# Kernel tuning notes

Measured on AMD Instinct MI355X. Metric: run time of the kernel, lower is better.

## Reference

```python
import jax, jax.numpy as jnp
import numpy as np

EPS = 1e-6

def _ln(x):
    mu = jnp.mean(x, -1, keepdims=True)
    var = jnp.mean((x - mu) ** 2, -1, keepdims=True)
    return (x - mu) / jnp.sqrt(var + EPS)

def _mha(q_in, k_in, v_in, w, mask, h):
    # w: [4, d, d] = (Wq, Wk, Wv, Wo), stored as [in, out]
    b, sq, d = q_in.shape
    dk = d // h
    q = (q_in @ w[0]).reshape(b, sq, h, dk)
    k = (k_in @ w[1]).reshape(b, k_in.shape[1], h, dk)
    v = (v_in @ w[2]).reshape(b, v_in.shape[1], h, dk)
    scores = jnp.einsum('bqhd,bkhd->bhqk', q, k) / np.sqrt(dk).astype(q.dtype)
    if mask is not None:
        scores = jnp.where(mask, scores, jnp.asarray(-jnp.inf, scores.dtype))
    attn = jax.nn.softmax(scores, -1)
    out = jnp.einsum('bhqk,bkhd->bqhd', attn, v).reshape(b, sq, d)
    return out @ w[3]

def setup_inputs() -> dict:
    B, S, D, V, NL, ML = 8, 256, 1024, 32000, 6, 256
    ks = jax.random.split(jax.random.key(0), 8)
    sc = 0.02
    return {
        'memory': jax.random.normal(ks[0], (B, S, D), jnp.float32),
        'gold_tokens': jax.random.randint(ks[1], (B, ML), 0, V),
        'attn_w': jax.random.normal(ks[2], (NL, 2, 4, D, D), jnp.float32) * sc,
        'ffn_w1': jax.random.normal(ks[3], (NL, D, 4 * D), jnp.float32) * sc,
        'ffn_w2': jax.random.normal(ks[4], (NL, 4 * D, D), jnp.float32) * sc,
        'tok_emb': jax.random.normal(ks[5], (V, D - ML), jnp.float32) * sc,
        'sos': jax.random.normal(ks[6], (D,), jnp.float32),
        'gen_w': jax.random.normal(ks[7], (D, V), jnp.float32) * sc,
    }

def reference(memory, gold_tokens, attn_w, ffn_w1, ffn_w2, tok_emb, sos, gen_w):
    B = memory.shape[0]
    ML = gold_tokens.shape[1]          # max_length == decoder len
    NL = attn_w.shape[0]
    H = 8
    temperature = 1.0
    # embedding: token embed (dim d-ML) concat one-hot position (dim ML)
    dec_input = gold_tokens[:, :-1]                      # [B, ML-1]
    tok = tok_emb[dec_input]                             # [B, ML-1, D-ML]
    pos = jax.nn.one_hot(jnp.arange(ML - 1), ML, dtype=tok.dtype)  # [ML-1, ML]
    pos = jnp.broadcast_to(pos[None], (B, ML - 1, ML))
    emb = jnp.concatenate([tok, pos], -1)                # [B, ML-1, D]
    sos_tok = jnp.broadcast_to(sos[None, None, :], (B, 1, sos.shape[0]))
    x = jnp.concatenate([sos_tok, emb], 1)               # [B, ML, D]
    causal = jnp.tril(jnp.ones((ML, ML), bool))[None, None]  # True = keep
    for l in range(NL):
        h1 = _ln(x)
        x = x + _mha(h1, h1, h1, attn_w[l, 0], causal, H)       # self-attn
        x = x + _mha(_ln(x), memory, memory, attn_w[l, 1], None, H)  # cross-attn (raw memory keys/values)
        h2 = _ln(x)
        x = x + jax.nn.relu(h2 @ ffn_w1[l]) @ ffn_w2[l]
    logits = _ln(x) @ gen_w
    return jax.nn.log_softmax(logits / temperature, -1)
```

## Files before the change

kernel.cpp:

```cpp
#include <hip/hip_runtime.h>
#include <hip/hip_bf16.h>
#include <cstdint>
#include <cstddef>

using bf16 = __hip_bfloat16;
typedef __attribute__((ext_vector_type(8))) short bf16x8;
typedef __attribute__((ext_vector_type(4))) float f32x4;

#define DEV static __device__ __forceinline__

DEV unsigned short f2bf(float f) {
    bf16 h = __float2bfloat16(f);
    return __builtin_bit_cast(unsigned short, h);
}

typedef const __attribute__((address_space(1))) void* as1cv;
typedef __attribute__((address_space(3))) void* as3v;

DEV void load_lds16(const void* g, void* l) {
    __builtin_amdgcn_global_load_lds((as1cv)g, (as3v)l, 16, 0, 0);
}

template<int EPI>
__global__ __launch_bounds__(256)
void gemm_k(const bf16* __restrict__ Ag, const bf16* __restrict__ Bg,
            void* __restrict__ Cg,
            int Mdim, int Ndim, int Kdim,
            int lda, int ldb, int ldc,
            int Hdim, long aZ1, long aZ2, long bZ1, long bZ2,
            long cZ1, long cZ2, float scale,
            float* __restrict__ pp, const bf16* __restrict__ Ag2, int ySplitA)
{
    __shared__ __align__(16) char lds[32768];
    char* ldsA = lds;
    char* ldsB = lds + 16384;

    const int t = threadIdx.x;
    const int wave = t >> 6, lane = t & 63;
    const int wr = wave >> 1, wc = wave & 1;
    const int lo = lane & 15, hi = lane >> 4;

    const int bx2 = blockIdx.x, by2 = blockIdx.y;
    const int m0 = bx2 * 128, n0 = by2 * 128;
    const int z = blockIdx.z;
    const int z1 = z / Hdim, z2 = z - z1 * Hdim;

    const bf16* Abase = (by2 >= ySplitA) ? Ag2 : Ag;
    const bf16* A = Abase + (size_t)z1 * aZ1 + (size_t)z2 * aZ2;
    const bf16* B = Bg + (size_t)z1 * bZ1 + (size_t)z2 * bZ2;

    f32x4 acc[4][4];
#pragma unroll
    for (int m = 0; m < 4; ++m)
#pragma unroll
        for (int n = 0; n < 4; ++n)
            acc[m][n] = f32x4{0.f, 0.f, 0.f, 0.f};

    const int nk = Kdim >> 6;
    for (int kt = 0; kt < nk; ++kt) {
        const int k0 = kt << 6;
#pragma unroll
        for (int i = 0; i < 4; ++i) {
            int u = i * 256 + t;
            int row = u >> 3;
            int cb = (u & 7) ^ (row & 7);
            load_lds16(A + (size_t)(m0 + row) * lda + (k0 + cb * 8),
                       ldsA + i * 4096 + wave * 1024);
        }
#pragma unroll
        for (int i = 0; i < 4; ++i) {
            int u = i * 256 + t;
            int row = u >> 3;
            int cb = (u & 7) ^ (row & 7);
            load_lds16(B + (size_t)(n0 + row) * ldb + (k0 + cb * 8),
                       ldsB + i * 4096 + wave * 1024);
        }
        __syncthreads();
#pragma unroll
        for (int kk = 0; kk < 2; ++kk) {
            bf16x8 af[4], bfr[4];
#pragma unroll
            for (int m = 0; m < 4; ++m) {
                int row = wr * 64 + m * 16 + lo;
                int cbyte = ((kk << 6) + (hi << 4)) ^ ((row & 7) << 4);
                af[m] = *(const bf16x8*)(ldsA + row * 128 + cbyte);
            }
#pragma unroll
            for (int n = 0; n < 4; ++n) {
                int row = wc * 64 + n * 16 + lo;
                int cbyte = ((kk << 6) + (hi << 4)) ^ ((row & 7) << 4);
                bfr[n] = *(const bf16x8*)(ldsB + row * 128 + cbyte);
            }
#pragma unroll
            for (int m = 0; m < 4; ++m)
#pragma unroll
                for (int n = 0; n < 4; ++n)
                    acc[m][n] = __builtin_amdgcn_mfma_f32_16x16x32_bf16(
                        af[m], bfr[n], acc[m][n], 0, 0, 0);
        }
        __syncthreads();
    }

    const int rb = hi << 2;
    if (EPI == 0 || EPI == 1) {
        unsigned short* C = (unsigned short*)Cg + (size_t)z1 * cZ1 + (size_t)z2 * cZ2;
#pragma unroll
        for (int m = 0; m < 4; ++m)
#pragma unroll
            for (int n = 0; n < 4; ++n)
#pragma unroll
                for (int r = 0; r < 4; ++r) {
                    int row = m0 + wr * 64 + m * 16 + rb + r;
                    int col = n0 + wc * 64 + n * 16 + lo;
                    float v = acc[m][n][r];
                    if (EPI == 1) v = fmaxf(v, 0.f);
                    C[(size_t)row * ldc + col] = f2bf(v);
                }
    } else if (EPI == 5) {
        float* C = (float*)Cg + (size_t)z1 * cZ1 + (size_t)z2 * cZ2;
#pragma unroll
        for (int m = 0; m < 4; ++m)
#pragma unroll
            for (int n = 0; n < 4; ++n)
#pragma unroll
                for (int r = 0; r < 4; ++r) {
                    int row = m0 + wr * 64 + m * 16 + rb + r;
                    int col = n0 + wc * 64 + n * 16 + lo;
                    atomicAdd(&C[(size_t)row * ldc + col], acc[m][n][r]);
                }
    } else {
        float* C = (float*)Cg + (size_t)z1 * cZ1 + (size_t)z2 * cZ2;
#pragma unroll
        for (int m = 0; m < 4; ++m)
#pragma unroll
            for (int n = 0; n < 4; ++n)
#pragma unroll
                for (int r = 0; r < 4; ++r) {
                    int row = m0 + wr * 64 + m * 16 + rb + r;
                    int col = n0 + wc * 64 + n * 16 + lo;
                    C[(size_t)row * ldc + col] = acc[m][n][r] * scale;
                }
        float* lp = (float*)lds;
#pragma unroll
        for (int m = 0; m < 4; ++m)
#pragma unroll
            for (int r = 0; r < 4; ++r) {
                float vm = -3.4e38f;
#pragma unroll
                for (int n = 0; n < 4; ++n) vm = fmaxf(vm, acc[m][n][r] * scale);
#pragma unroll
                for (int o = 1; o < 16; o <<= 1) vm = fmaxf(vm, __shfl_xor(vm, o));
                float vs = 0.f;
#pragma unroll
                for (int n = 0; n < 4; ++n) vs += __expf(acc[m][n][r] * scale - vm);
#pragma unroll
                for (int o = 1; o < 16; o <<= 1) vs += __shfl_xor(vs, o);
                if (lo == 0) {
                    int rl = wr * 64 + m * 16 + rb + r;
                    lp[(rl * 2 + wc) * 2 + 0] = vm;
                    lp[(rl * 2 + wc) * 2 + 1] = vs;
                }
            }
        __syncthreads();
        if (t < 128) {
            float ma = lp[(t * 2 + 0) * 2], sa = lp[(t * 2 + 0) * 2 + 1];
            float mb = lp[(t * 2 + 1) * 2], sb = lp[(t * 2 + 1) * 2 + 1];
            float mm = fmaxf(ma, mb);
            float ss = sa * __expf(ma - mm) + sb * __expf(mb - mm);
            size_t idx2 = ((size_t)(m0 + t) * gridDim.y + by2) * 2;
            pp[idx2] = mm; pp[idx2 + 1] = ss;
        }
    }
}

template<int CAUSAL>
__global__ __launch_bounds__(256)
void attn_k(const bf16* __restrict__ qkv, const bf16* __restrict__ VT,
            bf16* __restrict__ attno)
{
    __shared__ __align__(16) char ldsK[16384];
    __shared__ __align__(16) char ldsP[8192];
    const float SC = 0.088388347648318447f;

    const int t = threadIdx.x, w = t >> 6, lane = t & 63;
    const int lo = lane & 15, hi = lane >> 4;
    const int qb = blockIdx.x, z = blockIdx.y;
    const int b = z >> 3, h = z & 7;
    const int qr0 = qb * 64 + w * 16;

    const unsigned short* Qg = (const unsigned short*)qkv + (size_t)(b * 256) * 3072 + h * 128;
    const unsigned short* Kg = Qg + 1024;
    const unsigned short* VTz = (const unsigned short*)VT + (size_t)z * 32768;

    bf16x8 qf[4];
#pragma unroll
    for (int ks = 0; ks < 4; ++ks)
        qf[ks] = *(const bf16x8*)(Qg + (size_t)(qr0 + lo) * 3072 + ks * 32 + hi * 8);

    f32x4 accO[8];
#pragma unroll
    for (int n2 = 0; n2 < 8; ++n2) accO[n2] = f32x4{0.f, 0.f, 0.f, 0.f};
    float mrun[4], lrun[4];
#pragma unroll
    for (int r = 0; r < 4; ++r) { mrun[r] = -3.0e38f; lrun[r] = 0.f; }

    const int nkt = CAUSAL ? (qb + 1) : 4;
    for (int kt = 0; kt < nkt; ++kt) {
#pragma unroll
        for (int i = 0; i < 4; ++i) {
            int u = i * 256 + t;
            int row = u >> 4, j = u & 15;
            int sj = (j & 8) | ((j ^ row) & 7);
            load_lds16(Kg + (size_t)(kt * 64 + row) * 3072 + sj * 8,
                       ldsK + i * 4096 + w * 1024);
        }
        __syncthreads();

        f32x4 s4[4];
#pragma unroll
        for (int n = 0; n < 4; ++n) s4[n] = f32x4{0.f, 0.f, 0.f, 0.f};
#pragma unroll
        for (int ks = 0; ks < 4; ++ks)
#pragma unroll
            for (int n = 0; n < 4; ++n) {
                int kr = n * 16 + lo;
                int c = ks * 4 + hi;
                int sc2 = (c & 8) | ((c ^ (kr & 7)) & 7);
                bf16x8 kf = *(const bf16x8*)(ldsK + kr * 256 + sc2 * 16);
                s4[n] = __builtin_amdgcn_mfma_f32_16x16x32_bf16(qf[ks], kf, s4[n], 0, 0, 0);
            }

        float sv[4][4];
#pragma unroll
        for (int n = 0; n < 4; ++n)
#pragma unroll
            for (int r = 0; r < 4; ++r) {
                float v = s4[n][r] * SC;
                if (CAUSAL) {
                    int kg = kt * 64 + n * 16 + lo;
                    int qg2 = qb * 64 + w * 16 + hi * 4 + r;
                    if (kg > qg2) v = -3.0e38f;
                }
                sv[n][r] = v;
            }

        float sfv[4];
#pragma unroll
        for (int r = 0; r < 4; ++r) {
            float m2 = fmaxf(fmaxf(sv[0][r], sv[1][r]), fmaxf(sv[2][r], sv[3][r]));
#pragma unroll
            for (int o = 1; o < 16; o <<= 1) m2 = fmaxf(m2, __shfl_xor(m2, o));
            float mn = fmaxf(mrun[r], m2);
            sfv[r] = __expf(mrun[r] - mn);
            mrun[r] = mn;
        }
        float p[4][4], ts[4];
#pragma unroll
        for (int r = 0; r < 4; ++r) ts[r] = 0.f;
#pragma unroll
        for (int n = 0; n < 4; ++n)
#pragma unroll
            for (int r = 0; r < 4; ++r) {
                float e = __expf(sv[n][r] - mrun[r]);
                p[n][r] = e; ts[r] += e;
            }
#pragma unroll
        for (int r = 0; r < 4; ++r) {
            float s2 = ts[r];
#pragma unroll
            for (int o = 1; o < 16; o <<= 1) s2 += __shfl_xor(s2, o);
            lrun[r] = lrun[r] * sfv[r] + s2;
        }
#pragma unroll
        for (int n2 = 0; n2 < 8; ++n2)
#pragma unroll
            for (int r = 0; r < 4; ++r) accO[n2][r] *= sfv[r];

        char* pb = ldsP + w * 2048;
#pragma unroll
        for (int n = 0; n < 4; ++n)
#pragma unroll
            for (int r = 0; r < 4; ++r) {
                int q = hi * 4 + r, k = n * 16 + lo;
                int ch = (k >> 3) ^ (q & 7);
                *(unsigned short*)(pb + q * 128 + ch * 16 + (k & 7) * 2) = f2bf(p[n][r]);
            }
        __syncthreads();

#pragma unroll
        for (int ks2 = 0; ks2 < 2; ++ks2) {
            int c2 = (ks2 * 4 + hi) ^ (lo & 7);
            bf16x8 pa = *(const bf16x8*)(pb + lo * 128 + c2 * 16);
#pragma unroll
            for (int n2 = 0; n2 < 8; ++n2) {
                int d = n2 * 16 + lo;
                bf16x8 vb = *(const bf16x8*)(VTz + (size_t)d * 256 + kt * 64 + ks2 * 32 + hi * 8);
                accO[n2] = __builtin_amdgcn_mfma_f32_16x16x32_bf16(pa, vb, accO[n2], 0, 0, 0);
            }
        }
        __syncthreads();
    }

    float inv[4];
#pragma unroll
    for (int r = 0; r < 4; ++r) inv[r] = 1.f / lrun[r];
    unsigned short* Og = (unsigned short*)attno;
#pragma unroll
    for (int n2 = 0; n2 < 8; ++n2)
#pragma unroll
        for (int r = 0; r < 4; ++r) {
            int qg2 = qb * 64 + w * 16 + hi * 4 + r;
            int d = n2 * 16 + lo;
            Og[(size_t)(b * 256 + qg2) * 1024 + h * 128 + d] = f2bf(accO[n2][r] * inv[r]);
        }
}

DEV void wconv_tile(const float* __restrict__ W, unsigned short* __restrict__ WT,
                    int K, int N, int k0, int n0, int t, unsigned short* lds)
{
#pragma unroll
    for (int i = 0; i < 16; ++i) {
        int lin = i * 256 + t;
        int r = lin >> 6, c = lin & 63;
        lds[c * 65 + r] = f2bf(W[(size_t)(k0 + r) * N + n0 + c]);
    }
    __syncthreads();
#pragma unroll
    for (int i = 0; i < 16; ++i) {
        int lin = i * 256 + t;
        int r = lin >> 6, c = lin & 63;
        WT[(size_t)(n0 + r) * K + k0 + c] = lds[r * 65 + c];
    }
}

__global__ __launch_bounds__(256)
void wconv_k(const float* __restrict__ W, bf16* __restrict__ WT, int K, int N)
{
    __shared__ unsigned short lds[64 * 65];
    size_t moff = (size_t)blockIdx.z * K * N;
    wconv_tile(W + moff, (unsigned short*)WT + moff, K, N,
               blockIdx.x * 64, blockIdx.y * 64, threadIdx.x, lds);
}

__global__ __launch_bounds__(256)
void wconv3_k(const float* __restrict__ Wa, const float* __restrict__ W1,
              const float* __restrict__ W2, bf16* __restrict__ WTa,
              bf16* __restrict__ WT1, bf16* __restrict__ WT2)
{
    __shared__ unsigned short lds[64 * 65];
    int bid = blockIdx.x, t = threadIdx.x;
    if (bid < 2048) {
        int mat = bid >> 8, r = bid & 255;
        size_t moff = (size_t)mat * 1048576;
        wconv_tile(Wa + moff, (unsigned short*)WTa + moff, 1024, 1024,
                   (r & 15) * 64, (r >> 4) * 64, t, lds);
    } else if (bid < 3072) {
        int idx = bid - 2048;
        wconv_tile(W1, (unsigned short*)WT1, 1024, 4096,
                   (idx & 15) * 64, (idx >> 4) * 64, t, lds);
    } else {
        int idx = bid - 3072;
        wconv_tile(W2, (unsigned short*)WT2, 4096, 1024,
                   (idx & 63) * 64, (idx >> 6) * 64, t, lds);
    }
}

__global__ __launch_bounds__(256)
void f2b_k(const float* __restrict__ in, bf16* __restrict__ out, int n4)
{
    int i = blockIdx.x * 256 + threadIdx.x;
    if (i >= n4) return;
    float4 v = ((const float4*)in)[i];
    ushort4 o;
    o.x = f2bf(v.x); o.y = f2bf(v.y); o.z = f2bf(v.z); o.w = f2bf(v.w);
    ((ushort4*)out)[i] = o;
}

__global__ __launch_bounds__(256)
void embed_k(const float* __restrict__ tok_emb, const int* __restrict__ gold,
             const float* __restrict__ sos, float* __restrict__ x)
{
    int row = blockIdx.x;
    int b = row >> 8, sq = row & 255;
    int c4 = threadIdx.x;
    float4 v;
    if (sq == 0) {
        v = ((const float4*)sos)[c4];
    } else {
        int c = c4 << 2;
        if (c < 768) {
            int tok = gold[b * 256 + sq - 1];
            v = ((const float4*)(tok_emb + (size_t)tok * 768))[c4];
        } else {
            int p = sq - 1;
            v.x = (c + 0 - 768 == p) ? 1.f : 0.f;
            v.y = (c + 1 - 768 == p) ? 1.f : 0.f;
            v.z = (c + 2 - 768 == p) ? 1.f : 0.f;
            v.w = (c + 3 - 768 == p) ? 1.f : 0.f;
        }
    }
    ((float4*)(x + (size_t)row * 1024))[c4] = v;
}

__global__ __launch_bounds__(256)
void ln_k(const float* __restrict__ x, bf16* __restrict__ out)
{
    int row = blockIdx.x;
    const float4* xr = (const float4*)(x + (size_t)row * 1024);
    float4 v = xr[threadIdx.x];
    float s = v.x + v.y + v.z + v.w;
    float ss = v.x * v.x + v.y * v.y + v.z * v.z + v.w * v.w;
    for (int o = 32; o > 0; o >>= 1) { s += __shfl_down(s, o); ss += __shfl_down(ss, o); }
    __shared__ float buf[8];
    int wv = threadIdx.x >> 6;
    if ((threadIdx.x & 63) == 0) { buf[wv] = s; buf[4 + wv] = ss; }
    __syncthreads();
    float S = buf[0] + buf[1] + buf[2] + buf[3];
    float SS = buf[4] + buf[5] + buf[6] + buf[7];
    float mean = S * (1.f / 1024.f);
    float var = SS * (1.f / 1024.f) - mean * mean;
    float rstd = rsqrtf(var + 1e-6f);
    ushort4 o;
    o.x = f2bf((v.x - mean) * rstd);
    o.y = f2bf((v.y - mean) * rstd);
    o.z = f2bf((v.z - mean) * rstd);
    o.w = f2bf((v.w - mean) * rstd);
    ((ushort4*)out)[(size_t)row * 256 + threadIdx.x] = o;
}

__global__ __launch_bounds__(256)
void vtrans_k(const bf16* __restrict__ v, bf16* __restrict__ VT)
{
    __shared__ unsigned short lds[128 * 65];
    int z = blockIdx.y;
    int b = z >> 3, hh = z & 7;
    int sc = blockIdx.x;
    const unsigned short* src = (const unsigned short*)v
        + (size_t)(b * 256 + sc * 64) * 3072 + hh * 128;
    int t = threadIdx.x;
#pragma unroll
    for (int i = 0; i < 32; ++i) {
        int lin = i * 256 + t;
        int sl = lin >> 7, d = lin & 127;
        lds[d * 65 + sl] = src[(size_t)sl * 3072 + d];
    }
    __syncthreads();
    unsigned short* dst = (unsigned short*)VT + (size_t)z * 32768 + sc * 64;
#pragma unroll
    for (int i = 0; i < 32; ++i) {
        int lin = i * 256 + t;
        int d = lin >> 6, sl = lin & 63;
        dst[(size_t)d * 256 + sl] = lds[d * 65 + sl];
    }
}

__global__ __launch_bounds__(256)
void lsered_k(const float* __restrict__ pp, float* __restrict__ lse)
{
    const int NB = 250;
    int row = blockIdx.x, t = threadIdx.x;
    float m = -3.4e38f, s = 0.f;
    if (t < NB) {
        m = pp[((size_t)row * NB + t) * 2];
        s = pp[((size_t)row * NB + t) * 2 + 1];
    }
    for (int o = 32; o > 0; o >>= 1) {
        float om = __shfl_down(m, o), os = __shfl_down(s, o);
        float nm = fmaxf(m, om);
        s = s * __expf(m - nm) + os * __expf(om - nm);
        m = nm;
    }
    __shared__ float bm[4], bs[4];
    int wv = t >> 6;
    if ((t & 63) == 0) { bm[wv] = m; bs[wv] = s; }
    __syncthreads();
    if (t == 0) {
        float M = fmaxf(fmaxf(bm[0], bm[1]), fmaxf(bm[2], bm[3]));
        float S = bs[0] * __expf(bm[0] - M) + bs[1] * __expf(bm[1] - M)
                + bs[2] * __expf(bm[2] - M) + bs[3] * __expf(bm[3] - M);
        lse[row] = M + logf(S);
    }
}

__global__ __launch_bounds__(256)
void sub_k(float* __restrict__ out, const float* __restrict__ lse)
{
    size_t i = (size_t)blockIdx.x * 256 + threadIdx.x;
    float4* p = (float4*)out;
    float4 v = p[i];
    float L = lse[i / 8000];
    v.x -= L; v.y -= L; v.z -= L; v.w -= L;
    p[i] = v;
}

extern "C" void kernel_launch(void* const* d_in, const int* in_sizes, int n_in,
                              void* d_out, int out_size, void* d_ws, size_t ws_size,
                              hipStream_t stream)
{
    (void)in_sizes; (void)n_in; (void)out_size;
    const float* memory  = (const float*)d_in[0];
    const int*   gold    = (const int*)d_in[1];
    const float* attn_w  = (const float*)d_in[2];
    const float* ffn_w1  = (const float*)d_in[3];
    const float* ffn_w2  = (const float*)d_in[4];
    const float* tok_emb = (const float*)d_in[5];
    const float* sos     = (const float*)d_in[6];
    const float* gen_w   = (const float*)d_in[7];
    float* out = (float*)d_out;

    char* ws = (char*)d_ws;
    const size_t o_attnW = 0;
    const size_t o_ffn1W = o_attnW + 16777216;
    const size_t o_ffn2W = o_ffn1W + 8388608;
    const size_t o_qkv   = o_ffn2W + 8388608;
    const size_t o_attno = o_qkv + 12582912;
    const size_t o_tmp   = o_attno + 4194304;
    const size_t o_mem   = o_tmp + 29360128;
    const size_t o_x     = o_mem + 4194304;
    const size_t o_h     = o_x + 8388608;
    const size_t o_lse   = o_h + 4194304;
    const size_t NEEDED  = o_lse + 8192;
    if (ws_size < NEEDED) return;

    bf16*  attnWT = (bf16*)(ws + o_attnW);
    bf16*  ffn1WT = (bf16*)(ws + o_ffn1W);
    bf16*  ffn2WT = (bf16*)(ws + o_ffn2W);
    bf16*  qkv    = (bf16*)(ws + o_qkv);
    bf16*  attno  = (bf16*)(ws + o_attno);
    bf16*  VT     = (bf16*)(ws + o_tmp + 25165824);
    bf16*  ffnmid = (bf16*)(ws + o_tmp);
    bf16*  memb   = (bf16*)(ws + o_mem);
    float* x      = (float*)(ws + o_x);
    bf16*  h      = (bf16*)(ws + o_h);
    float* lse    = (float*)(ws + o_lse);
    float* parts  = (float*)(ws + o_mem);
    bf16*  genWT  = (bf16*)(ws + 0);

    const int BIG = 1 << 30;

    f2b_k<<<2048, 256, 0, stream>>>(memory, memb, 2048 * 1024 / 4);
    embed_k<<<2048, 256, 0, stream>>>(tok_emb, gold, sos, x);

    for (int l = 0; l < 6; ++l) {
        wconv3_k<<<4096, 256, 0, stream>>>(attn_w + (size_t)l * 8388608,
            ffn_w1 + (size_t)l * 4194304, ffn_w2 + (size_t)l * 4194304,
            attnWT, ffn1WT, ffn2WT);

        ln_k<<<2048, 256, 0, stream>>>(x, h);
        gemm_k<0><<<dim3(16,24,1), 256, 0, stream>>>(h, attnWT, qkv,
            2048, 3072, 1024, 1024, 1024, 3072, 1, 0,0,0,0,0,0, 0.f, nullptr, nullptr, BIG);
        vtrans_k<<<dim3(4,64), 256, 0, stream>>>(qkv + 2048, VT);
        attn_k<1><<<dim3(4,64), 256, 0, stream>>>(qkv, VT, attno);
        gemm_k<5><<<dim3(16,8,2), 256, 0, stream>>>(attno, attnWT + 3 * 1048576, x,
            2048, 1024, 512, 1024, 1024, 1024, 2, 0,512, 0,512, 0,0, 0.f, nullptr, nullptr, BIG);

        ln_k<<<2048, 256, 0, stream>>>(x, h);
        gemm_k<0><<<dim3(16,24,1), 256, 0, stream>>>(h, attnWT + 4 * 1048576, qkv,
            2048, 3072, 1024, 1024, 1024, 3072, 1, 0,0,0,0,0,0, 0.f, nullptr, memb, 8);
        vtrans_k<<<dim3(4,64), 256, 0, stream>>>(qkv + 2048, VT);
        attn_k<0><<<dim3(4,64), 256, 0, stream>>>(qkv, VT, attno);
        gemm_k<5><<<dim3(16,8,2), 256, 0, stream>>>(attno, attnWT + 7 * 1048576, x,
            2048, 1024, 512, 1024, 1024, 1024, 2, 0,512, 0,512, 0,0, 0.f, nullptr, nullptr, BIG);

        ln_k<<<2048, 256, 0, stream>>>(x, h);
        gemm_k<1><<<dim3(16,32,1), 256, 0, stream>>>(h, ffn1WT, ffnmid,
            2048, 4096, 1024, 1024, 1024, 4096, 1, 0,0,0,0,0,0, 0.f, nullptr, nullptr, BIG);
        gemm_k<5><<<dim3(16,8,4), 256, 0, stream>>>(ffnmid, ffn2WT, x,
            2048, 1024, 1024, 4096, 4096, 1024, 4, 0,1024, 0,1024, 0,0, 0.f, nullptr, nullptr, BIG);
    }

    wconv_k<<<dim3(16,500,1), 256, 0, stream>>>(gen_w, genWT, 1024, 32000);
    ln_k<<<2048, 256, 0, stream>>>(x, h);
    gemm_k<4><<<dim3(16,250,1), 256, 0, stream>>>(h, genWT, out,
        2048, 32000, 1024, 1024, 1024, 32000, 1, 0,0,0,0,0,0, 1.f, parts, nullptr, BIG);
    lsered_k<<<2048, 256, 0, stream>>>(parts, lse);
    sub_k<<<64000, 256, 0, stream>>>(out, lse);
}
```

Before: 1.752 ms.

## Double-buffer LDS tiles in GEMM and attention; fuse LSE reduce with subtract

The GEMM and attention kernels now use two LDS buffers. The next K tile's global-to-LDS loads are issued right after a single barrier, so they overlap with the MFMA work on the current tile, and one __syncthreads per iteration is removed. The log-softmax finish merges the LSE reduction and the subtract kernels into one per-row kernel, which saves a launch and an LSE round trip through global memory. In exchange, GEMM LDS grows to 64KB per block, which may cut occupancy. The attention kernel also drops a barrier around the per-wave P buffer, which relies on that buffer being wave-private.

```diff
diff --git a/kernel.cpp b/kernel.cpp
--- a/kernel.cpp
+++ b/kernel.cpp
@@ -31,9 +31,7 @@
             long cZ1, long cZ2, float scale,
             float* __restrict__ pp, const bf16* __restrict__ Ag2, int ySplitA)
 {
-    __shared__ __align__(16) char lds[32768];
-    char* ldsA = lds;
-    char* ldsB = lds + 16384;
+    __shared__ __align__(16) char lds[65536];
 
     const int t = threadIdx.x;
     const int wave = t >> 6, lane = t & 63;
@@ -57,15 +55,18 @@
             acc[m][n] = f32x4{0.f, 0.f, 0.f, 0.f};
 
     const int nk = Kdim >> 6;
-    for (int kt = 0; kt < nk; ++kt) {
+
+    auto stage = [&](int kt, int buf) {
         const int k0 = kt << 6;
+        char* dA = lds + buf * 32768;
+        char* dB = dA + 16384;
 #pragma unroll
         for (int i = 0; i < 4; ++i) {
             int u = i * 256 + t;
             int row = u >> 3;
             int cb = (u & 7) ^ (row & 7);
             load_lds16(A + (size_t)(m0 + row) * lda + (k0 + cb * 8),
-                       ldsA + i * 4096 + wave * 1024);
+                       dA + i * 4096 + wave * 1024);
         }
 #pragma unroll
         for (int i = 0; i < 4; ++i) {
@@ -73,9 +74,17 @@
             int row = u >> 3;
             int cb = (u & 7) ^ (row & 7);
             load_lds16(B + (size_t)(n0 + row) * ldb + (k0 + cb * 8),
-                       ldsB + i * 4096 + wave * 1024);
-        }
+                       dB + i * 4096 + wave * 1024);
+        }
+    };
+
+    stage(0, 0);
+    int cur = 0;
+    for (int kt = 0; kt < nk; ++kt) {
         __syncthreads();
+        if (kt + 1 < nk) stage(kt + 1, cur ^ 1);
+        char* ldsA = lds + cur * 32768;
+        char* ldsB = ldsA + 16384;
 #pragma unroll
         for (int kk = 0; kk < 2; ++kk) {
             bf16x8 af[4], bfr[4];
@@ -98,7 +107,7 @@
                     acc[m][n] = __builtin_amdgcn_mfma_f32_16x16x32_bf16(
                         af[m], bfr[n], acc[m][n], 0, 0, 0);
         }
-        __syncthreads();
+        cur ^= 1;
     }
 
     const int rb = hi << 2;
@@ -140,6 +149,7 @@
                     int col = n0 + wc * 64 + n * 16 + lo;
                     C[(size_t)row * ldc + col] = acc[m][n][r] * scale;
                 }
+        __syncthreads();
         float* lp = (float*)lds;
 #pragma unroll
         for (int m = 0; m < 4; ++m)
@@ -178,7 +188,7 @@
 void attn_k(const bf16* __restrict__ qkv, const bf16* __restrict__ VT,
             bf16* __restrict__ attno)
 {
-    __shared__ __align__(16) char ldsK[16384];
+    __shared__ __align__(16) char ldsK[2][16384];
     __shared__ __align__(16) char ldsP[8192];
     const float SC = 0.088388347648318447f;
 
@@ -204,17 +214,23 @@
 #pragma unroll
     for (int r = 0; r < 4; ++r) { mrun[r] = -3.0e38f; lrun[r] = 0.f; }
 
-    const int nkt = CAUSAL ? (qb + 1) : 4;
-    for (int kt = 0; kt < nkt; ++kt) {
+    auto stageK = [&](int kt, int buf) {
 #pragma unroll
         for (int i = 0; i < 4; ++i) {
             int u = i * 256 + t;
             int row = u >> 4, j = u & 15;
             int sj = (j & 8) | ((j ^ row) & 7);
             load_lds16(Kg + (size_t)(kt * 64 + row) * 3072 + sj * 8,
-                       ldsK + i * 4096 + w * 1024);
-        }
+                       ldsK[buf] + i * 4096 + w * 1024);
+        }
+    };
+
+    const int nkt = CAUSAL ? (qb + 1) : 4;
+    stageK(0, 0);
+    int cur = 0;
+    for (int kt = 0; kt < nkt; ++kt) {
         __syncthreads();
+        if (kt + 1 < nkt) stageK(kt + 1, cur ^ 1);
 
         f32x4 s4[4];
 #pragma unroll
@@ -226,7 +242,7 @@
                 int kr = n * 16 + lo;
                 int c = ks * 4 + hi;
                 int sc2 = (c & 8) | ((c ^ (kr & 7)) & 7);
-                bf16x8 kf = *(const bf16x8*)(ldsK + kr * 256 + sc2 * 16);
+                bf16x8 kf = *(const bf16x8*)(ldsK[cur] + kr * 256 + sc2 * 16);
                 s4[n] = __builtin_amdgcn_mfma_f32_16x16x32_bf16(qf[ks], kf, s4[n], 0, 0, 0);
             }
 
@@ -285,7 +301,6 @@
                 int ch = (k >> 3) ^ (q & 7);
                 *(unsigned short*)(pb + q * 128 + ch * 16 + (k & 7) * 2) = f2bf(p[n][r]);
             }
-        __syncthreads();
 
 #pragma unroll
         for (int ks2 = 0; ks2 < 2; ++ks2) {
@@ -298,7 +313,7 @@
                 accO[n2] = __builtin_amdgcn_mfma_f32_16x16x32_bf16(pa, vb, accO[n2], 0, 0, 0);
             }
         }
-        __syncthreads();
+        cur ^= 1;
     }
 
     float inv[4];
@@ -455,7 +470,7 @@
 }
 
 __global__ __launch_bounds__(256)
-void lsered_k(const float* __restrict__ pp, float* __restrict__ lse)
+void lsesub_k(float* __restrict__ out, const float* __restrict__ pp)
 {
     const int NB = 250;
     int row = blockIdx.x, t = threadIdx.x;
@@ -471,6 +486,7 @@
         m = nm;
     }
     __shared__ float bm[4], bs[4];
+    __shared__ float sL;
     int wv = t >> 6;
     if ((t & 63) == 0) { bm[wv] = m; bs[wv] = s; }
     __syncthreads();
@@ -478,19 +494,16 @@
         float M = fmaxf(fmaxf(bm[0], bm[1]), fmaxf(bm[2], bm[3]));
         float S = bs[0] * __expf(bm[0] - M) + bs[1] * __expf(bm[1] - M)
                 + bs[2] * __expf(bm[2] - M) + bs[3] * __expf(bm[3] - M);
-        lse[row] = M + logf(S);
-    }
-}
-
-__global__ __launch_bounds__(256)
-void sub_k(float* __restrict__ out, const float* __restrict__ lse)
-{
-    size_t i = (size_t)blockIdx.x * 256 + threadIdx.x;
-    float4* p = (float4*)out;
-    float4 v = p[i];
-    float L = lse[i / 8000];
-    v.x -= L; v.y -= L; v.z -= L; v.w -= L;
-    p[i] = v;
+        sL = M + logf(S);
+    }
+    __syncthreads();
+    float L = sL;
+    float4* p = (float4*)(out + (size_t)row * 32000);
+    for (int i = t; i < 8000; i += 256) {
+        float4 v = p[i];
+        v.x -= L; v.y -= L; v.z -= L; v.w -= L;
+        p[i] = v;
+    }
 }
 
 extern "C" void kernel_launch(void* const* d_in, const int* in_sizes, int n_in,
@@ -532,7 +545,6 @@
     bf16*  memb   = (bf16*)(ws + o_mem);
     float* x      = (float*)(ws + o_x);
     bf16*  h      = (bf16*)(ws + o_h);
-    float* lse    = (float*)(ws + o_lse);
     float* parts  = (float*)(ws + o_mem);
     bf16*  genWT  = (bf16*)(ws + 0);
 
@@ -573,6 +585,5 @@
     ln_k<<<2048, 256, 0, stream>>>(x, h);
     gemm_k<4><<<dim3(16,250,1), 256, 0, stream>>>(h, genWT, out,
         2048, 32000, 1024, 1024, 1024, 32000, 1, 0,0,0,0,0,0, 1.f, parts, nullptr, BIG);
-    lsered_k<<<2048, 256, 0, stream>>>(parts, lse);
-    sub_k<<<64000, 256, 0, stream>>>(out, lse);
-}
+    lsesub_k<<<2048, 256, 0, stream>>>(out, parts);
+}
```

Result: faster. 1.668 ms (-4.8%).
